# Kernel tuning notes

Measured on AMD Instinct MI355X. Metric: run time of the kernel, lower is better.

The kernel has to match this reference:

```python
import jax, jax.numpy as jnp
import numpy as np

H, D, G = 8, 64, 64          # num_heads, head_dim, num_slices
HID = H * D                  # 512
EPS = 1e-5
N = 100000


def setup_inputs() -> dict:
    key = jax.random.key(0)
    ks = jax.random.split(key, 16)
    s = 0.02  # init scale
    return {
        "x": jax.random.normal(ks[0], (N, HID), dtype=jnp.float32),
        # x_proj / fx_proj: Linear(HID -> HID) with bias, eqx stores W as (out, in)
        "Wx": jax.random.normal(ks[1], (HID, HID), dtype=jnp.float32) * s,
        "bx": jax.random.normal(ks[2], (HID,), dtype=jnp.float32) * s,
        "Wfx": jax.random.normal(ks[3], (HID, HID), dtype=jnp.float32) * s,
        "bfx": jax.random.normal(ks[4], (HID,), dtype=jnp.float32) * s,
        # slice_proj: Linear(D -> G) with bias
        "Ws": jax.random.normal(ks[5], (G, D), dtype=jnp.float32) * s,
        "bs": jax.random.normal(ks[6], (G,), dtype=jnp.float32) * s,
        # learned temperature, init 0.5, shape (H,1,1)
        "temperature": jnp.ones((H, 1, 1), dtype=jnp.float32) * 0.5,
        # slice MultiheadAttention (num_heads=1, size D): q/k/v/out proj, no biases (eqx defaults)
        "Wq": jax.random.normal(ks[7], (D, D), dtype=jnp.float32) * s,
        "Wk": jax.random.normal(ks[8], (D, D), dtype=jnp.float32) * s,
        "Wv": jax.random.normal(ks[9], (D, D), dtype=jnp.float32) * s,
        "Wo": jax.random.normal(ks[10], (D, D), dtype=jnp.float32) * s,
        # out_proj: Linear(HID -> HID) with bias
        "Wout": jax.random.normal(ks[11], (HID, HID), dtype=jnp.float32) * s,
        "bout": jax.random.normal(ks[12], (HID,), dtype=jnp.float32) * s,
    }


def reference(x, Wx, bx, Wfx, bfx, Ws, bs, temperature, Wq, Wk, Wv, Wo, Wout, bout):
    n = x.shape[0]
    # token projections, split into heads: (H, N, D)
    x_mid = (x @ Wx.T + bx).reshape(n, H, D).transpose(1, 0, 2)
    fx_mid = (x @ Wfx.T + bfx).reshape(n, H, D).transpose(1, 0, 2)

    # slice weights: proj -> temperature-scaled softmax over G  (H, N, G)
    logits = jnp.einsum('hnd,gd->hng', x_mid, Ws) + bs
    w = jax.nn.softmax(logits * temperature, axis=-1)

    # weighted pooling to slice tokens (H, G, D)
    norm = w.sum(axis=1)                                   # (H, G)
    tokens = jnp.einsum('hnd,hng->hgd', fx_mid, w) / (norm[..., None] + EPS)

    # small single-head attention over the G slice tokens, vmapped over H
    q = jnp.einsum('hgd,od->hgo', tokens, Wq)
    k = jnp.einsum('hgd,od->hgo', tokens, Wk)
    v = jnp.einsum('hgd,od->hgo', tokens, Wv)
    attn = jax.nn.softmax(jnp.einsum('hgd,hkd->hgk', q, k) / jnp.sqrt(jnp.float32(D)), axis=-1)
    out_tok = jnp.einsum('hgk,hkd->hgd', attn, v)
    out_tok = jnp.einsum('hgd,od->hgo', out_tok, Wo)

    # deslice: weighted unpooling back to tokens, merge heads, output projection
    out = jnp.einsum('hgd,hng->hnd', out_tok, w)           # (H, N, D)
    out = out.transpose(1, 0, 2).reshape(n, HID)
    return out @ Wout.T + bout
```

## Files before the change

### kernel.cpp

```cpp
#include <hip/hip_runtime.h>
#include <hip/hip_bf16.h>

#define HID 512
#define NH  8
#define DD  64
#define GG  64
#define EPSF 1e-5f

typedef __attribute__((ext_vector_type(8))) short short8;
typedef __attribute__((ext_vector_type(4))) float floatx4;

__device__ __forceinline__ short f2bf(float f) {
    union { float f; unsigned u; } v; v.f = f;
    unsigned r = v.u + 0x7fffu + ((v.u >> 16) & 1u);
    return (short)(r >> 16);
}
__device__ __forceinline__ float bf2f(short s) {
    union { unsigned u; float f; } v;
    v.u = ((unsigned)(unsigned short)s) << 16;
    return v.f;
}

#define GLOAD_LDS16(g, l) __builtin_amdgcn_global_load_lds( \
    (const __attribute__((address_space(1))) unsigned int*)(g), \
    (__attribute__((address_space(3))) unsigned int*)(l), 16, 0, 0)

__global__ __launch_bounds__(256)
void cast_kernel(const float* __restrict__ x, short* __restrict__ xb, int n8) {
    int i = blockIdx.x * 256 + threadIdx.x;
    if (i >= n8) return;
    const float4* p = (const float4*)(x + (size_t)i * 8);
    float4 a = p[0], b = p[1];
    short8 v;
    v[0] = f2bf(a.x); v[1] = f2bf(a.y); v[2] = f2bf(a.z); v[3] = f2bf(a.w);
    v[4] = f2bf(b.x); v[5] = f2bf(b.y); v[6] = f2bf(b.z); v[7] = f2bf(b.w);
    *(short8*)(xb + (size_t)i * 8) = v;
}

__global__ void fold1_kernel(const float* __restrict__ Wx, const float* __restrict__ bx,
                             const float* __restrict__ Wfx, const float* __restrict__ bfx,
                             const float* __restrict__ Ws, const float* __restrict__ bs,
                             const float* __restrict__ temp,
                             short* __restrict__ Wcat, float* __restrict__ bias_cat) {
    int idx = blockIdx.x * 256 + threadIdx.x;
    int row = idx >> 9;
    int k = idx & 511;
    float val;
    if (row < 512) {
        val = Wfx[row * 512 + k];
        if (k == 0) bias_cat[row] = bfx[row];
    } else {
        int hg = row - 512;
        int h = hg >> 6, g = hg & 63;
        float t = temp[h];
        float s = 0.f;
        #pragma unroll 8
        for (int d = 0; d < 64; ++d) s += Ws[g * 64 + d] * Wx[(h * 64 + d) * 512 + k];
        val = s * t;
        if (k == 0) {
            float b = 0.f;
            for (int d = 0; d < 64; ++d) b += Ws[g * 64 + d] * bx[h * 64 + d];
            bias_cat[row] = (b + bs[g]) * t;
        }
    }
    Wcat[idx] = f2bf(val);
}

template <bool OUT_F32, bool FUSE_SM>
__global__ __launch_bounds__(512, 2)
void gemm256(const short* __restrict__ A, int lda,
             const short* __restrict__ B,
             const float* __restrict__ bias,
             void* __restrict__ Cp, int ldc,
             int M, int clog2, int Rtiles) {
    __shared__ short As[2][256 * 64];
    __shared__ short Bs[2][256 * 64];

    const int id = blockIdx.x;
    const int xcd = id & 7;
    const int s = id >> 3;
    const int cblk = s & ((1 << clog2) - 1);
    const int slice = (Rtiles + 7) >> 3;
    const int rt = xcd * slice + (s >> clog2);
    if (rt >= Rtiles) return;

    const int tid = threadIdx.x;
    const int wid = tid >> 6;
    const int lane = tid & 63;
    const int wm = wid >> 2, wn = wid & 3;
    const int lr = lane & 15, lq = lane >> 4;
    const int row0 = rt * 256, col0 = cblk * 256;

    const int srow = tid >> 3;
    const int schunk = (tid & 7) ^ (srow & 7);
    const short* Asrc = A + (size_t)(row0 + srow) * lda + schunk * 8;
    const short* Bsrc = B + (size_t)(col0 + srow) * lda + schunk * 8;
    const int ldst = wid * 512;

#define SA(buf, kt, Lk) GLOAD_LDS16(Asrc + (size_t)((Lk) * 64) * lda + (kt) * 64, \
                                    &As[buf][(Lk) * 4096 + ldst])
#define SB(buf, kt, Lk) GLOAD_LDS16(Bsrc + (size_t)((Lk) * 64) * lda + (kt) * 64, \
                                    &Bs[buf][(Lk) * 4096 + ldst])

    const int axor = lr & 7;
    const int coff0 = (lq ^ axor) * 8;
    const int coff1 = ((4 + lq) ^ axor) * 8;
    const int aoff = (wm * 128 + lr) * 64;
    const int boff = (wn * 64 + lr) * 64;

    floatx4 acc[8][4];
    #pragma unroll
    for (int i = 0; i < 8; ++i)
        #pragma unroll
        for (int j = 0; j < 4; ++j) acc[i][j] = (floatx4)(0.f);

    SA(0, 0, 0); SA(0, 0, 1); SA(0, 0, 2); SA(0, 0, 3);
    SB(0, 0, 0); SB(0, 0, 1); SB(0, 0, 2); SB(0, 0, 3);
    SB(1, 1, 0); SB(1, 1, 1); SB(1, 1, 2); SB(1, 1, 3);
    SA(1, 1, 0); SA(1, 1, 2);
    asm volatile("s_waitcnt vmcnt(6)" ::: "memory");
    __builtin_amdgcn_s_barrier();

    short8 bfr[4][2];
    short8 af[2][2];

    #pragma unroll 1
    for (int u = 0; u < 4; ++u) {
        const int st = (u < 3);
        #pragma unroll
        for (int cb = 0; cb < 2; ++cb) {
            #pragma unroll
            for (int p = 0; p < 4; ++p) {
                const int q = cb * 4 + p;
                if (p == 0) {
                    #pragma unroll
                    for (int j = 0; j < 4; ++j) {
                        bfr[j][0] = *(const short8*)&Bs[cb][boff + j * 1024 + coff0];
                        bfr[j][1] = *(const short8*)&Bs[cb][boff + j * 1024 + coff1];
                    }
                }
                #pragma unroll
                for (int i2 = 0; i2 < 2; ++i2) {
                    af[i2][0] = *(const short8*)&As[cb][aoff + (2 * p + i2) * 1024 + coff0];
                    af[i2][1] = *(const short8*)&As[cb][aoff + (2 * p + i2) * 1024 + coff1];
                }
                if (q == 0)      { SA(1, 2 * u + 1, 1); SA(1, 2 * u + 1, 3); }
                else if (st) {
                    if (q == 1)      { SB(0, 2 * u + 2, 0); SB(0, 2 * u + 2, 1); }
                    else if (q == 2) { SB(0, 2 * u + 2, 2); SB(0, 2 * u + 2, 3); }
                    else if (q == 3) { SA(0, 2 * u + 2, 0); SA(0, 2 * u + 2, 2); }
                    else if (q == 4) { SA(0, 2 * u + 2, 1); SA(0, 2 * u + 2, 3); }
                    else if (q == 5) { SB(1, 2 * u + 3, 0); SB(1, 2 * u + 3, 1); }
                    else if (q == 6) { SB(1, 2 * u + 3, 2); SB(1, 2 * u + 3, 3); }
                    else             { SA(1, 2 * u + 3, 0); SA(1, 2 * u + 3, 2); }
                }
                if (q == 3) {
                    if (st) asm volatile("s_waitcnt vmcnt(6)" ::: "memory");
                    else    asm volatile("s_waitcnt vmcnt(0)" ::: "memory");
                } else if (q == 7 && st) {
                    asm volatile("s_waitcnt vmcnt(6)" ::: "memory");
                }
                __builtin_amdgcn_s_barrier();
                __builtin_amdgcn_s_setprio(1);
                #pragma unroll
                for (int ks = 0; ks < 2; ++ks)
                    #pragma unroll
                    for (int i2 = 0; i2 < 2; ++i2)
                        #pragma unroll
                        for (int j = 0; j < 4; ++j)
                            acc[2 * p + i2][j] = __builtin_amdgcn_mfma_f32_16x16x32_bf16(
                                af[i2][ks], bfr[j][ks], acc[2 * p + i2][j], 0, 0, 0);
                __builtin_amdgcn_s_setprio(0);
                __builtin_amdgcn_s_barrier();
            }
        }
    }
#undef SA
#undef SB

    float bcol[4];
    #pragma unroll
    for (int j = 0; j < 4; ++j) bcol[j] = bias[col0 + wn * 64 + j * 16 + lr];

    const bool do_sm = FUSE_SM && (col0 >= 512);
    #pragma unroll
    for (int i = 0; i < 8; ++i) {
        #pragma unroll
        for (int r = 0; r < 4; ++r) {
            const int grow = row0 + wm * 128 + i * 16 + lq * 4 + r;
            float v[4];
            #pragma unroll
            for (int j = 0; j < 4; ++j) v[j] = acc[i][j][r] + bcol[j];
            if (do_sm) {
                float m = fmaxf(fmaxf(v[0], v[1]), fmaxf(v[2], v[3]));
                #pragma unroll
                for (int off = 1; off < 16; off <<= 1) m = fmaxf(m, __shfl_xor(m, off));
                float sum = 0.f;
                #pragma unroll
                for (int j = 0; j < 4; ++j) { v[j] = __expf(v[j] - m); sum += v[j]; }
                #pragma unroll
                for (int off = 1; off < 16; off <<= 1) sum += __shfl_xor(sum, off);
                const float inv = 1.f / sum;
                #pragma unroll
                for (int j = 0; j < 4; ++j) v[j] *= inv;
            }
            if (grow < M) {
                #pragma unroll
                for (int j = 0; j < 4; ++j) {
                    const int gcol = col0 + wn * 64 + j * 16 + lr;
                    if constexpr (OUT_F32) ((float*)Cp)[(size_t)grow * ldc + gcol] = v[j];
                    else                   ((short*)Cp)[(size_t)grow * ldc + gcol] = f2bf(v[j]);
                }
            }
        }
    }
}

__global__ __launch_bounds__(256)
void pool_mfma(const short* __restrict__ mid, float* __restrict__ tok_raw,
               float* __restrict__ norm, int N, int chunk) {
    const int h = blockIdx.y;
    const int n0 = blockIdx.x * chunk;
    if (n0 >= N) return;
    const int ksteps = (min(chunk, N - n0)) >> 5;

    const int tid = threadIdx.x;
    const int wid = tid >> 6, lane = tid & 63;
    const int lr = lane & 15, lq = lane >> 4;
    const int wg = (wid >> 1) * 32, wd = (wid & 1) * 32;

    __shared__ short wt[32 * 72];
    __shared__ short ft[32 * 72];

    const int sn = tid >> 3;
    const int sc0 = (tid & 7) * 8;
    const int scr = (sc0 + 16 * ((sn >> 3) & 3)) & 63;
    const int st_off = sn * 72 + scr;

    const int ra = ((wg + lr) + 16 * lq) & 63;
    const int rb = ((wd + lr) + 16 * lq) & 63;

    const short* wbase = mid + (size_t)n0 * 1024 + 512 + h * 64;
    const short* fbase = mid + (size_t)n0 * 1024 + h * 64;

    floatx4 acc[2][2];
    #pragma unroll
    for (int i = 0; i < 2; ++i)
        #pragma unroll
        for (int j = 0; j < 2; ++j) acc[i][j] = (floatx4)(0.f);
    floatx4 accn[2];
    accn[0] = (floatx4)(0.f); accn[1] = (floatx4)(0.f);

    short8 ones;
    #pragma unroll
    for (int j = 0; j < 8; ++j) ones[j] = (short)0x3F80;

    for (int ks = 0; ks < ksteps; ++ks) {
        const size_t roff = (size_t)(ks * 32 + sn) * 1024;
        short8 wv = *(const short8*)(wbase + roff + sc0);
        short8 fv = *(const short8*)(fbase + roff + sc0);
        __syncthreads();
        *(short8*)&wt[st_off] = wv;
        *(short8*)&ft[st_off] = fv;
        __syncthreads();

        short8 af[2], bf_[2];
        #pragma unroll
        for (int i = 0; i < 2; ++i) {
            short tmpv[8];
            #pragma unroll
            for (int j = 0; j < 8; ++j)
                tmpv[j] = wt[(lq * 8 + j) * 72 + ((ra + i * 16) & 63)];
            af[i] = *(const short8*)tmpv;
        }
        #pragma unroll
        for (int j2 = 0; j2 < 2; ++j2) {
            short tmpv[8];
            #pragma unroll
            for (int j = 0; j < 8; ++j)
                tmpv[j] = ft[(lq * 8 + j) * 72 + ((rb + j2 * 16) & 63)];
            bf_[j2] = *(const short8*)tmpv;
        }
        #pragma unroll
        for (int i = 0; i < 2; ++i)
            #pragma unroll
            for (int j = 0; j < 2; ++j)
                acc[i][j] = __builtin_amdgcn_mfma_f32_16x16x32_bf16(af[i], bf_[j], acc[i][j], 0, 0, 0);
        if (wd == 0) {
            #pragma unroll
            for (int i = 0; i < 2; ++i)
                accn[i] = __builtin_amdgcn_mfma_f32_16x16x32_bf16(af[i], ones, accn[i], 0, 0, 0);
        }
    }

    #pragma unroll
    for (int i = 0; i < 2; ++i) {
        #pragma unroll
        for (int r = 0; r < 4; ++r) {
            int g = wg + i * 16 + lq * 4 + r;
            #pragma unroll
            for (int j = 0; j < 2; ++j) {
                int d = wd + j * 16 + lr;
                atomicAdd(&tok_raw[(h * 64 + g) * 64 + d], acc[i][j][r]);
            }
        }
    }
    if (wd == 0 && lr == 0) {
        #pragma unroll
        for (int i = 0; i < 2; ++i)
            #pragma unroll
            for (int r = 0; r < 4; ++r)
                atomicAdd(&norm[h * 64 + wg + i * 16 + lq * 4 + r], accn[i][r]);
    }
}

__global__ __launch_bounds__(256)
void attn_kernel(const float* __restrict__ tok_raw, const float* __restrict__ norm,
                 const float* __restrict__ Wq, const float* __restrict__ Wk,
                 const float* __restrict__ Wv, const float* __restrict__ Wo,
                 float* __restrict__ out_tok) {
    const int h = blockIdx.x;
    const int tid = threadIdx.x;
    const int g = tid & 63, part = tid >> 6;
    const int o0 = part * 16;

    __shared__ float tk[64][65];
    __shared__ float qq[64][65];
    __shared__ float kk[64][65];
    __shared__ float vv[64][65];
    __shared__ float pp[64][65];
    __shared__ float od[64][65];

    const float inv = 1.f / (norm[h * 64 + g] + EPSF);
    #pragma unroll
    for (int dd = 0; dd < 16; ++dd) {
        int d = o0 + dd;
        tk[g][d] = tok_raw[(size_t)(h * 64 + g) * 64 + d] * inv;
    }
    __syncthreads();

    float t[64];
    #pragma unroll
    for (int d = 0; d < 64; ++d) t[d] = tk[g][d];
    #pragma unroll
    for (int oo = 0; oo < 16; ++oo) {
        int o = o0 + oo;
        float sq = 0.f, sk = 0.f, sv = 0.f;
        #pragma unroll
        for (int d = 0; d < 64; ++d) {
            float td = t[d];
            sq += td * Wq[o * 64 + d];
            sk += td * Wk[o * 64 + d];
            sv += td * Wv[o * 64 + d];
        }
        qq[g][o] = sq; kk[g][o] = sk; vv[g][o] = sv;
    }
    __syncthreads();

    float q[64];
    #pragma unroll
    for (int o = 0; o < 64; ++o) q[o] = qq[g][o];
    #pragma unroll
    for (int jj = 0; jj < 16; ++jj) {
        int j = o0 + jj;
        float s = 0.f;
        #pragma unroll
        for (int o = 0; o < 64; ++o) s += q[o] * kk[j][o];
        pp[g][j] = s * 0.125f;
    }
    __syncthreads();

    float sr[64];
    float mx = -1e30f;
    #pragma unroll
    for (int j = 0; j < 64; ++j) { sr[j] = pp[g][j]; mx = fmaxf(mx, sr[j]); }
    float sum = 0.f;
    #pragma unroll
    for (int j = 0; j < 64; ++j) { sr[j] = __expf(sr[j] - mx); sum += sr[j]; }
    const float isum = 1.f / sum;

    #pragma unroll
    for (int dd = 0; dd < 16; ++dd) {
        int d = o0 + dd;
        float a = 0.f;
        #pragma unroll
        for (int j = 0; j < 64; ++j) a += sr[j] * vv[j][d];
        od[g][d] = a * isum;
    }
    __syncthreads();

    float ot[64];
    #pragma unroll
    for (int d = 0; d < 64; ++d) ot[d] = od[g][d];
    #pragma unroll
    for (int oo = 0; oo < 16; ++oo) {
        int o = o0 + oo;
        float a = 0.f;
        #pragma unroll
        for (int d = 0; d < 64; ++d) a += ot[d] * Wo[o * 64 + d];
        out_tok[(size_t)(h * 64 + g) * 64 + o] = a;
    }
}

__global__ void fold2_kernel(const float* __restrict__ out_tok,
                             const float* __restrict__ Wout, short* __restrict__ Vbf) {
    int idx = blockIdx.x * 256 + threadIdx.x;
    int o = idx >> 9, hg = idx & 511;
    int h = hg >> 6;
    const float* ot = out_tok + (size_t)hg * 64;
    const float* wo = Wout + (size_t)o * 512 + h * 64;
    float s = 0.f;
    #pragma unroll 8
    for (int d = 0; d < 64; ++d) s += ot[d] * wo[d];
    Vbf[idx] = f2bf(s);
}

extern "C" void kernel_launch(void* const* d_in, const int* in_sizes, int n_in,
                              void* d_out, int out_size, void* d_ws, size_t ws_size,
                              hipStream_t stream) {
    const float* x    = (const float*)d_in[0];
    const float* Wx   = (const float*)d_in[1];
    const float* bx   = (const float*)d_in[2];
    const float* Wfx  = (const float*)d_in[3];
    const float* bfx  = (const float*)d_in[4];
    const float* Ws   = (const float*)d_in[5];
    const float* bs   = (const float*)d_in[6];
    const float* temp = (const float*)d_in[7];
    const float* Wq   = (const float*)d_in[8];
    const float* Wk   = (const float*)d_in[9];
    const float* Wv   = (const float*)d_in[10];
    const float* Wo   = (const float*)d_in[11];
    const float* Wout = (const float*)d_in[12];
    const float* bout = (const float*)d_in[13];

    const int N = in_sizes[0] / HID;

    char* p = (char*)d_ws;
    short* mid = (short*)p;           p += (size_t)N * 1024 * 2;
    short* Wcat = (short*)p;          p += (size_t)1024 * 512 * 2;
    float* bias_cat = (float*)p;      p += 1024 * 4;
    float* tok_raw = (float*)p;       p += (size_t)NH * GG * DD * 4;
    float* norm_ = (float*)p;         p += (size_t)NH * GG * 4;
    float* out_tok = (float*)p;       p += (size_t)NH * GG * DD * 4;
    short* Vbf = (short*)p;           p += (size_t)512 * 512 * 2;
    short* x_bf = (short*)d_out;

    cast_kernel<<<(N * 512 / 8 + 255) / 256, 256, 0, stream>>>(x, x_bf, N * 512 / 8);
    fold1_kernel<<<2048, 256, 0, stream>>>(Wx, bx, Wfx, bfx, Ws, bs, temp, Wcat, bias_cat);

    const int R = (N + 255) / 256;
    const int slice = (R + 7) / 8;

    gemm256<false, true><<<8 * slice * 4, 512, 0, stream>>>(
        x_bf, HID, Wcat, bias_cat, (void*)mid, 1024, N, 2, R);

    hipMemsetAsync(tok_raw, 0, (size_t)(NH * GG * DD + NH * GG) * 4, stream);

    const int chunk = 544;
    dim3 g2((N + chunk - 1) / chunk, 8);
    pool_mfma<<<g2, 256, 0, stream>>>(mid, tok_raw, norm_, N, chunk);

    attn_kernel<<<8, 256, 0, stream>>>(tok_raw, norm_, Wq, Wk, Wv, Wo, out_tok);

    fold2_kernel<<<1024, 256, 0, stream>>>(out_tok, Wout, Vbf);

    gemm256<true, false><<<8 * slice * 2, 512, 0, stream>>>(
        mid + 512, 1024, Vbf, bout, d_out, HID, N, 1, R);
}
```

Measured before the change: 813.8 us.

## Make GEMM kernels persistent with cross-tile prefetch of next A tile

```diff
diff --git a/kernel.cpp b/kernel.cpp
--- a/kernel.cpp
+++ b/kernel.cpp
@@ -66,40 +66,43 @@
     Wcat[idx] = f2bf(val);
 }
 
-template <bool OUT_F32, bool FUSE_SM>
+template <bool OUT_F32, bool FUSE_SM, int CB>
 __global__ __launch_bounds__(512, 2)
-void gemm256(const short* __restrict__ A, int lda,
-             const short* __restrict__ B,
-             const float* __restrict__ bias,
-             void* __restrict__ Cp, int ldc,
-             int M, int clog2, int Rtiles) {
+void gemm256p(const short* __restrict__ A, int lda,
+              const short* __restrict__ B,
+              const float* __restrict__ bias,
+              void* __restrict__ Cp, int ldc,
+              int M, int RperX, int Rtiles) {
     __shared__ short As[2][256 * 64];
     __shared__ short Bs[2][256 * 64];
 
-    const int id = blockIdx.x;
-    const int xcd = id & 7;
-    const int s = id >> 3;
-    const int cblk = s & ((1 << clog2) - 1);
-    const int slice = (Rtiles + 7) >> 3;
-    const int rt = xcd * slice + (s >> clog2);
-    if (rt >= Rtiles) return;
+    const int bid = blockIdx.x;
+    const int xcd = bid & 7;
+    const int q_  = bid >> 3;
+    const int cb  = q_ % CB;
+    const int u0  = q_ / CB;
+    const int STEP = 32 / CB;
+    const int cnt = (RperX - u0 + STEP - 1) / STEP;
+    if (cnt <= 0) return;
 
     const int tid = threadIdx.x;
     const int wid = tid >> 6;
     const int lane = tid & 63;
     const int wm = wid >> 2, wn = wid & 3;
     const int lr = lane & 15, lq = lane >> 4;
-    const int row0 = rt * 256, col0 = cblk * 256;
+    const int col0 = cb * 256;
 
     const int srow = tid >> 3;
     const int schunk = (tid & 7) ^ (srow & 7);
-    const short* Asrc = A + (size_t)(row0 + srow) * lda + schunk * 8;
     const short* Bsrc = B + (size_t)(col0 + srow) * lda + schunk * 8;
+    int rt = xcd * RperX + u0;
+    const int soff = srow * lda + schunk * 8;
+    const short* Ac = A + (size_t)min(rt, Rtiles - 1) * 256 * lda + soff;
     const int ldst = wid * 512;
 
-#define SA(buf, kt, Lk) GLOAD_LDS16(Asrc + (size_t)((Lk) * 64) * lda + (kt) * 64, \
-                                    &As[buf][(Lk) * 4096 + ldst])
-#define SB(buf, kt, Lk) GLOAD_LDS16(Bsrc + (size_t)((Lk) * 64) * lda + (kt) * 64, \
+#define GA(buf, base, kt, Lk) GLOAD_LDS16((base) + (size_t)((Lk) * 64) * lda + (kt) * 64, \
+                                          &As[buf][(Lk) * 4096 + ldst])
+#define GB(buf, kt, Lk) GLOAD_LDS16(Bsrc + (size_t)((Lk) * 64) * lda + (kt) * 64, \
                                     &Bs[buf][(Lk) * 4096 + ldst])
 
     const int axor = lr & 7;
@@ -108,16 +111,21 @@
     const int aoff = (wm * 128 + lr) * 64;
     const int boff = (wn * 64 + lr) * 64;
 
+    float bcol[4];
+    #pragma unroll
+    for (int j = 0; j < 4; ++j) bcol[j] = bias[col0 + wn * 64 + j * 16 + lr];
+    const bool do_sm = FUSE_SM && (cb >= CB / 2);
+
     floatx4 acc[8][4];
     #pragma unroll
     for (int i = 0; i < 8; ++i)
         #pragma unroll
         for (int j = 0; j < 4; ++j) acc[i][j] = (floatx4)(0.f);
 
-    SA(0, 0, 0); SA(0, 0, 1); SA(0, 0, 2); SA(0, 0, 3);
-    SB(0, 0, 0); SB(0, 0, 1); SB(0, 0, 2); SB(0, 0, 3);
-    SB(1, 1, 0); SB(1, 1, 1); SB(1, 1, 2); SB(1, 1, 3);
-    SA(1, 1, 0); SA(1, 1, 2);
+    GA(0, Ac, 0, 0); GA(0, Ac, 0, 1); GA(0, Ac, 0, 2); GA(0, Ac, 0, 3);
+    GB(0, 0, 0); GB(0, 0, 1); GB(0, 0, 2); GB(0, 0, 3);
+    GB(1, 1, 0); GB(1, 1, 1); GB(1, 1, 2); GB(1, 1, 3);
+    GA(1, Ac, 1, 0); GA(1, Ac, 1, 2);
     asm volatile("s_waitcnt vmcnt(6)" ::: "memory");
     __builtin_amdgcn_s_barrier();
 
@@ -125,95 +133,102 @@
     short8 af[2][2];
 
     #pragma unroll 1
-    for (int u = 0; u < 4; ++u) {
-        const int st = (u < 3);
-        #pragma unroll
-        for (int cb = 0; cb < 2; ++cb) {
-            #pragma unroll
-            for (int p = 0; p < 4; ++p) {
-                const int q = cb * 4 + p;
-                if (p == 0) {
+    for (int t = 0; t < cnt; ++t) {
+        const short* An = (t + 1 < cnt)
+            ? (A + (size_t)min(rt + STEP, Rtiles - 1) * 256 * lda + soff)
+            : Ac;
+
+        #pragma unroll 1
+        for (int u = 0; u < 4; ++u) {
+            const short* Au = (u == 3) ? An : Ac;
+            const int ku1 = 2 * u + 1;
+            const int kt2 = (2 * u + 2) & 7, kt3 = (2 * u + 3) & 7;
+            #pragma unroll
+            for (int cbuf = 0; cbuf < 2; ++cbuf) {
+                #pragma unroll
+                for (int p = 0; p < 4; ++p) {
+                    const int q = cbuf * 4 + p;
+                    if (p == 0) {
+                        #pragma unroll
+                        for (int j = 0; j < 4; ++j) {
+                            bfr[j][0] = *(const short8*)&Bs[cbuf][boff + j * 1024 + coff0];
+                            bfr[j][1] = *(const short8*)&Bs[cbuf][boff + j * 1024 + coff1];
+                        }
+                    }
+                    #pragma unroll
+                    for (int i2 = 0; i2 < 2; ++i2) {
+                        af[i2][0] = *(const short8*)&As[cbuf][aoff + (2 * p + i2) * 1024 + coff0];
+                        af[i2][1] = *(const short8*)&As[cbuf][aoff + (2 * p + i2) * 1024 + coff1];
+                    }
+                    if (q == 0)      { GA(1, Ac, ku1, 1); GA(1, Ac, ku1, 3); }
+                    else if (q == 1) { GB(0, kt2, 0); GB(0, kt2, 1); }
+                    else if (q == 2) { GB(0, kt2, 2); GB(0, kt2, 3); }
+                    else if (q == 3) { GA(0, Au, kt2, 0); GA(0, Au, kt2, 2); }
+                    else if (q == 4) { GA(0, Au, kt2, 1); GA(0, Au, kt2, 3); }
+                    else if (q == 5) { GB(1, kt3, 0); GB(1, kt3, 1); }
+                    else if (q == 6) { GB(1, kt3, 2); GB(1, kt3, 3); }
+                    else             { GA(1, Au, kt3, 0); GA(1, Au, kt3, 2); }
+                    if (q == 3 || q == 7)
+                        asm volatile("s_waitcnt vmcnt(6)" ::: "memory");
+                    __builtin_amdgcn_s_barrier();
+                    __builtin_amdgcn_s_setprio(1);
+                    #pragma unroll
+                    for (int ks = 0; ks < 2; ++ks)
+                        #pragma unroll
+                        for (int i2 = 0; i2 < 2; ++i2)
+                            #pragma unroll
+                            for (int j = 0; j < 4; ++j)
+                                acc[2 * p + i2][j] = __builtin_amdgcn_mfma_f32_16x16x32_bf16(
+                                    af[i2][ks], bfr[j][ks], acc[2 * p + i2][j], 0, 0, 0);
+                    __builtin_amdgcn_s_setprio(0);
+                    __builtin_amdgcn_s_barrier();
+                }
+            }
+        }
+
+        const int row0 = rt * 256;
+        #pragma unroll
+        for (int i = 0; i < 8; ++i) {
+            #pragma unroll
+            for (int r = 0; r < 4; ++r) {
+                const int grow = row0 + wm * 128 + i * 16 + lq * 4 + r;
+                float v[4];
+                #pragma unroll
+                for (int j = 0; j < 4; ++j) v[j] = acc[i][j][r] + bcol[j];
+                if (do_sm) {
+                    float m = fmaxf(fmaxf(v[0], v[1]), fmaxf(v[2], v[3]));
+                    #pragma unroll
+                    for (int off = 1; off < 16; off <<= 1) m = fmaxf(m, __shfl_xor(m, off));
+                    float sum = 0.f;
+                    #pragma unroll
+                    for (int j = 0; j < 4; ++j) { v[j] = __expf(v[j] - m); sum += v[j]; }
+                    #pragma unroll
+                    for (int off = 1; off < 16; off <<= 1) sum += __shfl_xor(sum, off);
+                    const float inv = 1.f / sum;
+                    #pragma unroll
+                    for (int j = 0; j < 4; ++j) v[j] *= inv;
+                }
+                if (grow < M) {
                     #pragma unroll
                     for (int j = 0; j < 4; ++j) {
-                        bfr[j][0] = *(const short8*)&Bs[cb][boff + j * 1024 + coff0];
-                        bfr[j][1] = *(const short8*)&Bs[cb][boff + j * 1024 + coff1];
+                        const int gcol = col0 + wn * 64 + j * 16 + lr;
+                        if constexpr (OUT_F32) ((float*)Cp)[(size_t)grow * ldc + gcol] = v[j];
+                        else                   ((short*)Cp)[(size_t)grow * ldc + gcol] = f2bf(v[j]);
                     }
                 }
-                #pragma unroll
-                for (int i2 = 0; i2 < 2; ++i2) {
-                    af[i2][0] = *(const short8*)&As[cb][aoff + (2 * p + i2) * 1024 + coff0];
-                    af[i2][1] = *(const short8*)&As[cb][aoff + (2 * p + i2) * 1024 + coff1];
-                }
-                if (q == 0)      { SA(1, 2 * u + 1, 1); SA(1, 2 * u + 1, 3); }
-                else if (st) {
-                    if (q == 1)      { SB(0, 2 * u + 2, 0); SB(0, 2 * u + 2, 1); }
-                    else if (q == 2) { SB(0, 2 * u + 2, 2); SB(0, 2 * u + 2, 3); }
-                    else if (q == 3) { SA(0, 2 * u + 2, 0); SA(0, 2 * u + 2, 2); }
-                    else if (q == 4) { SA(0, 2 * u + 2, 1); SA(0, 2 * u + 2, 3); }
-                    else if (q == 5) { SB(1, 2 * u + 3, 0); SB(1, 2 * u + 3, 1); }
-                    else if (q == 6) { SB(1, 2 * u + 3, 2); SB(1, 2 * u + 3, 3); }
-                    else             { SA(1, 2 * u + 3, 0); SA(1, 2 * u + 3, 2); }
-                }
-                if (q == 3) {
-                    if (st) asm volatile("s_waitcnt vmcnt(6)" ::: "memory");
-                    else    asm volatile("s_waitcnt vmcnt(0)" ::: "memory");
-                } else if (q == 7 && st) {
-                    asm volatile("s_waitcnt vmcnt(6)" ::: "memory");
-                }
-                __builtin_amdgcn_s_barrier();
-                __builtin_amdgcn_s_setprio(1);
-                #pragma unroll
-                for (int ks = 0; ks < 2; ++ks)
-                    #pragma unroll
-                    for (int i2 = 0; i2 < 2; ++i2)
-                        #pragma unroll
-                        for (int j = 0; j < 4; ++j)
-                            acc[2 * p + i2][j] = __builtin_amdgcn_mfma_f32_16x16x32_bf16(
-                                af[i2][ks], bfr[j][ks], acc[2 * p + i2][j], 0, 0, 0);
-                __builtin_amdgcn_s_setprio(0);
-                __builtin_amdgcn_s_barrier();
             }
         }
-    }
-#undef SA
-#undef SB
-
-    float bcol[4];
-    #pragma unroll
-    for (int j = 0; j < 4; ++j) bcol[j] = bias[col0 + wn * 64 + j * 16 + lr];
-
-    const bool do_sm = FUSE_SM && (col0 >= 512);
-    #pragma unroll
-    for (int i = 0; i < 8; ++i) {
-        #pragma unroll
-        for (int r = 0; r < 4; ++r) {
-            const int grow = row0 + wm * 128 + i * 16 + lq * 4 + r;
-            float v[4];
-            #pragma unroll
-            for (int j = 0; j < 4; ++j) v[j] = acc[i][j][r] + bcol[j];
-            if (do_sm) {
-                float m = fmaxf(fmaxf(v[0], v[1]), fmaxf(v[2], v[3]));
-                #pragma unroll
-                for (int off = 1; off < 16; off <<= 1) m = fmaxf(m, __shfl_xor(m, off));
-                float sum = 0.f;
-                #pragma unroll
-                for (int j = 0; j < 4; ++j) { v[j] = __expf(v[j] - m); sum += v[j]; }
-                #pragma unroll
-                for (int off = 1; off < 16; off <<= 1) sum += __shfl_xor(sum, off);
-                const float inv = 1.f / sum;
-                #pragma unroll
-                for (int j = 0; j < 4; ++j) v[j] *= inv;
-            }
-            if (grow < M) {
-                #pragma unroll
-                for (int j = 0; j < 4; ++j) {
-                    const int gcol = col0 + wn * 64 + j * 16 + lr;
-                    if constexpr (OUT_F32) ((float*)Cp)[(size_t)grow * ldc + gcol] = v[j];
-                    else                   ((short*)Cp)[(size_t)grow * ldc + gcol] = f2bf(v[j]);
-                }
-            }
-        }
-    }
+        #pragma unroll
+        for (int i = 0; i < 8; ++i)
+            #pragma unroll
+            for (int j = 0; j < 4; ++j) acc[i][j] = (floatx4)(0.f);
+
+        Ac = An;
+        rt += STEP;
+    }
+#undef GA
+#undef GB
+    asm volatile("s_waitcnt vmcnt(0) lgkmcnt(0)" ::: "memory");
 }
 
 __global__ __launch_bounds__(256)
@@ -449,10 +464,10 @@
     fold1_kernel<<<2048, 256, 0, stream>>>(Wx, bx, Wfx, bfx, Ws, bs, temp, Wcat, bias_cat);
 
     const int R = (N + 255) / 256;
-    const int slice = (R + 7) / 8;
-
-    gemm256<false, true><<<8 * slice * 4, 512, 0, stream>>>(
-        x_bf, HID, Wcat, bias_cat, (void*)mid, 1024, N, 2, R);
+    const int RperX = (R + 7) / 8;
+
+    gemm256p<false, true, 4><<<256, 512, 0, stream>>>(
+        x_bf, HID, Wcat, bias_cat, (void*)mid, 1024, N, RperX, R);
 
     hipMemsetAsync(tok_raw, 0, (size_t)(NH * GG * DD + NH * GG) * 4, stream);
 
@@ -464,6 +479,6 @@
 
     fold2_kernel<<<1024, 256, 0, stream>>>(out_tok, Wout, Vbf);
 
-    gemm256<true, false><<<8 * slice * 2, 512, 0, stream>>>(
-        mid + 512, 1024, Vbf, bout, d_out, HID, N, 1, R);
-}
+    gemm256p<true, false, 2><<<256, 512, 0, stream>>>(
+        mid + 512, 1024, Vbf, bout, d_out, HID, N, RperX, R);
+}
```

After: 886.3 us. +8.9%, slower.
